# Kernel tuning notes

Measured on AMD Instinct MI355X. Metric: run time of the kernel, lower is better.

The kernel has to match this reference:

```python
import jax, jax.numpy as jnp
import numpy as np

BN_EPS = 1e-5


def setup_inputs() -> dict:
    key = jax.random.key(0)
    k_x, k_A, k_W, k_b = jax.random.split(key, 4)
    N, C_in, T, V = 32, 64, 300, 25
    P, C_out = 3, 128
    x = jax.random.normal(k_x, (N, C_in, T, V), dtype=jnp.float32)
    # adjacency partitions: nonnegative, row-normalized-ish (rand in [0,1))
    A = jax.random.uniform(k_A, (P, V, V), dtype=jnp.float32)
    # kaiming fan_in init for 1x1 conv weights: std = sqrt(2/fan_in)
    W = jax.random.normal(k_W, (P, C_out, C_in), dtype=jnp.float32) * np.sqrt(2.0 / C_in)
    b = jax.random.normal(k_b, (P, C_out), dtype=jnp.float32) * 0.01
    gamma = jnp.ones((C_out,), dtype=jnp.float32)
    beta = jnp.zeros((C_out,), dtype=jnp.float32)
    return {"x": x, "A": A, "W": W, "b": b, "gamma": gamma, "beta": beta}


def reference(x, A, W, b, gamma, beta):
    # x: (N, C, T, V); A: (P, V, V); W: (P, C_out, C_in); b: (P, C_out)
    # Per partition p: aggregate over graph (x @ A_p), then 1x1 conv, then sum over p.
    # Fused: y[n,o,t,v] = sum_p sum_c W[p,o,c] * (sum_w x[n,c,t,w] * A[p,w,v]) + sum_p b[p,o]
    xa = jnp.einsum('nctw,pwv->pnctv', x, A)            # (P, N, C_in, T, V)
    y = jnp.einsum('pnctv,poc->notv', xa, W)            # (N, C_out, T, V)
    y = y + jnp.sum(b, axis=0)[None, :, None, None]
    # BatchNorm2d, training-mode forward: stats over (N, T, V), biased variance
    mean = jnp.mean(y, axis=(0, 2, 3), keepdims=True)
    var = jnp.mean(jnp.square(y - mean), axis=(0, 2, 3), keepdims=True)
    y = (y - mean) * jax.lax.rsqrt(var + BN_EPS)
    y = y * gamma[None, :, None, None] + beta[None, :, None, None]
    return jax.nn.relu(y)
```

## Files before the change

kernel.cpp:

```cpp
#include <hip/hip_runtime.h>
#include <hip/hip_bf16.h>

#define NN 32
#define CIN 64
#define TTOT 300
#define VV 25
#define PP 3
#define COUT 128
#define TTILE 5
#define NTILES 60
#define CNT 240000.0f

#define XSTR 40
#define ZSTR 72
#define ZROWS 128

#define WS_STATS 0
#define WS_SCALE 256
#define WS_SHIFT 384
#define WS_BSUM  512
#define WS_W2    640

typedef float f32x4 __attribute__((ext_vector_type(4)));
typedef short s16x8 __attribute__((ext_vector_type(8)));

__device__ __forceinline__ short f2bf(float f) {
    unsigned u = __float_as_uint(f);
    u += 0x7fff + ((u >> 16) & 1);
    return (short)(u >> 16);
}

__global__ __launch_bounds__(256) void prep_kernel(const float* __restrict__ W,
                                                   const float* __restrict__ b,
                                                   float* __restrict__ ws) {
    int tid = blockIdx.x * blockDim.x + threadIdx.x;
    if (tid < 256) ws[WS_STATS + tid] = 0.0f;
    if (tid >= 256 && tid < 384) {
        int o = tid - 256;
        ws[WS_BSUM + o] = b[o] + b[COUT + o] + b[2 * COUT + o];
    }
    if (tid < COUT * 192) {
        int o = tid / 192, k = tid % 192;
        int p = k / 64, c = k % 64;
        ((short*)(ws + WS_W2))[tid] = f2bf(W[(p * COUT + o) * CIN + c]);
    }
}

__global__ __launch_bounds__(512, 4) void sgcn_main(const float* __restrict__ x,
                                                    const float* __restrict__ A,
                                                    float* __restrict__ y,
                                                    float* ws) {
    __shared__ __align__(16) short Xs[TTILE * 64 * XSTR];
    __shared__ __align__(16) short Ats[PP * 32 * XSTR];
    __shared__ __align__(16) short Z2s[ZROWS * ZSTR];
    __shared__ float sstat[256];
    const int tid  = threadIdx.x;
    const int lane = tid & 63;
    const int wave = tid >> 6;
    const int n  = blockIdx.x / NTILES;
    const int t0 = (blockIdx.x % NTILES) * TTILE;
    const int lg = lane >> 4;
    const int li = lane & 15;

    {
        const float* xb = x + (size_t)n * (CIN * TTOT * VV) + (size_t)t0 * VV;
        #pragma unroll
        for (int it = 0; it < 20; ++it) {
            int i = tid + it * 512;
            int c = i / 160;
            int r2 = i - c * 160;
            int t = r2 >> 5, w = r2 & 31;
            float val = (w < VV) ? xb[c * (TTOT * VV) + t * VV + w] : 0.0f;
            Xs[(t * 64 + c) * XSTR + w] = f2bf(val);
        }
        #pragma unroll
        for (int it = 0; it < 8; ++it) {
            int i = tid + it * 512;
            if (i < PP * 32 * XSTR) {
                int p = i / (32 * XSTR);
                int r = i - p * (32 * XSTR);
                int v = r / XSTR, w = r - v * XSTR;
                short val = (v < VV && w < VV) ? f2bf(A[p * (VV * VV) + w * VV + v])
                                               : (short)0;
                Ats[i] = val;
            }
        }
        if (tid < 108) ((int*)(Z2s + 125 * ZSTR))[tid] = 0;
        if (tid < 256) sstat[tid] = 0.0f;
    }
    __syncthreads();

    const int ow = wave >> 1;
    const int cw = wave & 1;
    const int o0 = ow * 32;
    const short* w2 = (const short*)(ws + WS_W2);

    f32x4 acc[2][4];
    #pragma unroll
    for (int mf = 0; mf < 2; ++mf)
        #pragma unroll
        for (int cf = 0; cf < 4; ++cf)
            acc[mf][cf] = (f32x4){0.f, 0.f, 0.f, 0.f};

    for (int p = 0; p < PP; ++p) {
        s16x8 wf[2][2];
        #pragma unroll
        for (int mf = 0; mf < 2; ++mf)
            #pragma unroll
            for (int ks = 0; ks < 2; ++ks)
                wf[mf][ks] = *(const s16x8*)(w2 + (o0 + mf * 16 + li) * 192
                                                + p * 64 + ks * 32 + lg * 8);

        #pragma unroll
        for (int q = 0; q < 5; ++q) {
            int f = wave * 5 + q;
            int t = f >> 3, rem = f & 7;
            int vf = rem >> 2, cfr = rem & 3;
            s16x8 af = *(const s16x8*)(&Ats[(p * 32 + vf * 16 + li) * XSTR + lg * 8]);
            s16x8 bf = *(const s16x8*)(&Xs[(t * 64 + cfr * 16 + li) * XSTR + lg * 8]);
            f32x4 z = (f32x4){0.f, 0.f, 0.f, 0.f};
            f32x4 d = __builtin_amdgcn_mfma_f32_16x16x32_bf16(af, bf, z, 0, 0, 0);
            int m0 = vf * 16 + lg * 4;
            int ccol = cfr * 16 + li;
            #pragma unroll
            for (int r = 0; r < 4; ++r) {
                int m = m0 + r;
                if (m < VV) Z2s[(t * VV + m) * ZSTR + ccol] = f2bf(d[r]);
            }
        }
        __syncthreads();

        #pragma unroll
        for (int cf = 0; cf < 4; ++cf) {
            int col0 = cw * 64 + cf * 16;
            #pragma unroll
            for (int ks = 0; ks < 2; ++ks) {
                s16x8 zf = *(const s16x8*)(&Z2s[(col0 + li) * ZSTR + ks * 32 + lg * 8]);
                #pragma unroll
                for (int mf = 0; mf < 2; ++mf)
                    acc[mf][cf] = __builtin_amdgcn_mfma_f32_16x16x32_bf16(
                        wf[mf][ks], zf, acc[mf][cf], 0, 0, 0);
            }
        }
        __syncthreads();
    }

    const float* bsum = ws + WS_BSUM;
    #pragma unroll
    for (int mf = 0; mf < 2; ++mf) {
        #pragma unroll
        for (int r = 0; r < 4; ++r) {
            int o = o0 + mf * 16 + lg * 4 + r;
            float bo = bsum[o];
            float s = 0.f, sq = 0.f;
            #pragma unroll
            for (int cf = 0; cf < 4; ++cf) {
                int col = cw * 64 + cf * 16 + li;
                float val = acc[mf][cf][r] + bo;
                if (col < TTILE * VV) {
                    y[(size_t)(n * COUT + o) * (TTOT * VV) + t0 * VV + col] = val;
                    s += val; sq += val * val;
                }
            }
            #pragma unroll
            for (int m = 1; m < 16; m <<= 1) {
                s  += __shfl_xor(s, m, 64);
                sq += __shfl_xor(sq, m, 64);
            }
            if (li == 0) {
                atomicAdd(&sstat[o], s);
                atomicAdd(&sstat[128 + o], sq);
            }
        }
    }
    __syncthreads();
    if (tid < 256) atomicAdd(&ws[WS_STATS + tid], sstat[tid]);
}

__global__ void finalize_kernel(const float* __restrict__ gamma,
                                const float* __restrict__ beta,
                                float* ws) {
    int o = threadIdx.x;
    float mean = ws[WS_STATS + o] * (1.0f / CNT);
    float ex2  = ws[WS_STATS + 128 + o] * (1.0f / CNT);
    float var  = ex2 - mean * mean;
    float rstd = rsqrtf(var + 1e-5f);
    float sc = gamma[o] * rstd;
    ws[WS_SCALE + o] = sc;
    ws[WS_SHIFT + o] = beta[o] - mean * sc;
}

__global__ __launch_bounds__(256) void norm_relu_kernel(float* __restrict__ y,
                                                        const float* __restrict__ ws) {
    const int total8 = (NN * COUT * TTOT * VV) / 8;
    const float* scale = ws + WS_SCALE;
    const float* shift = ws + WS_SHIFT;
    for (int i = blockIdx.x * blockDim.x + threadIdx.x; i < total8;
         i += gridDim.x * blockDim.x) {
        size_t base = (size_t)i * 8;
        int row0 = (int)(base / 7500);
        int row1 = (int)((base + 7) / 7500);
        int o0 = row0 & 127, o1 = row1 & 127;
        float s0 = scale[o0], h0 = shift[o0];
        float s1 = scale[o1], h1 = shift[o1];
        size_t bnd = (size_t)(row0 + 1) * 7500;
        float4 a = *(const float4*)(y + base);
        float4 b = *(const float4*)(y + base + 4);
        float vals[8] = {a.x, a.y, a.z, a.w, b.x, b.y, b.z, b.w};
        #pragma unroll
        for (int e = 0; e < 8; ++e) {
            bool first = (base + (size_t)e) < bnd;
            float s = first ? s0 : s1;
            float h = first ? h0 : h1;
            vals[e] = fmaxf(vals[e] * s + h, 0.0f);
        }
        a = make_float4(vals[0], vals[1], vals[2], vals[3]);
        b = make_float4(vals[4], vals[5], vals[6], vals[7]);
        *(float4*)(y + base) = a;
        *(float4*)(y + base + 4) = b;
    }
}

extern "C" void kernel_launch(void* const* d_in, const int* in_sizes, int n_in,
                              void* d_out, int out_size, void* d_ws, size_t ws_size,
                              hipStream_t stream) {
    const float* x     = (const float*)d_in[0];
    const float* A     = (const float*)d_in[1];
    const float* W     = (const float*)d_in[2];
    const float* b     = (const float*)d_in[3];
    const float* gamma = (const float*)d_in[4];
    const float* beta  = (const float*)d_in[5];
    float* y  = (float*)d_out;
    float* ws = (float*)d_ws;

    prep_kernel<<<96, 256, 0, stream>>>(W, b, ws);
    sgcn_main<<<NN * NTILES, 512, 0, stream>>>(x, A, y, ws);
    finalize_kernel<<<1, 128, 0, stream>>>(gamma, beta, ws);
    norm_relu_kernel<<<2048, 256, 0, stream>>>(y, ws);
}
```

Baseline: 148.6 us.

## Split fused graph-aggregation/conv kernel into two kernels through a bf16 workspace

Replaces the single fused kernel with an aggregation kernel that writes the x·A result as a bf16 column-major buffer (K=192 contiguous per column) into workspace, followed by a conv kernel that loads 128 columns via direct global-to-LDS loads with an XOR swizzle and runs a K=192 MFMA GEMM against preloaded weights. The intent is to drop the per-partition barriers and the low-utilisation 125-column tiles of the fused kernel, giving full 128-column tiles with all weights held in registers. In exchange it adds a round trip of roughly 92 MB of intermediate traffic, and it only takes effect when the workspace is large enough, falling back to the old kernel otherwise.

```diff
diff --git a/kernel.cpp b/kernel.cpp
--- a/kernel.cpp
+++ b/kernel.cpp
@@ -7,9 +7,11 @@
 #define VV 25
 #define PP 3
 #define COUT 128
+#define KTOT 192
 #define TTILE 5
 #define NTILES 60
 #define CNT 240000.0f
+#define NCOLS 240000
 
 #define XSTR 40
 #define ZSTR 72
@@ -20,6 +22,8 @@
 #define WS_SHIFT 384
 #define WS_BSUM  512
 #define WS_W2    640
+#define ZT_BYTE_OFF (1u << 20)
+#define WS_NEEDED (ZT_BYTE_OFF + (size_t)NCOLS * KTOT * 2)
 
 typedef float f32x4 __attribute__((ext_vector_type(4)));
 typedef short s16x8 __attribute__((ext_vector_type(8)));
@@ -28,6 +32,12 @@
     unsigned u = __float_as_uint(f);
     u += 0x7fff + ((u >> 16) & 1);
     return (short)(u >> 16);
+}
+
+__device__ __forceinline__ void gl_lds16(const void* g, void* l) {
+    __builtin_amdgcn_global_load_lds(
+        (const __attribute__((address_space(1))) unsigned int*)g,
+        (__attribute__((address_space(3))) unsigned int*)l, 16, 0, 0);
 }
 
 __global__ __launch_bounds__(256) void prep_kernel(const float* __restrict__ W,
@@ -39,10 +49,176 @@
         int o = tid - 256;
         ws[WS_BSUM + o] = b[o] + b[COUT + o] + b[2 * COUT + o];
     }
-    if (tid < COUT * 192) {
-        int o = tid / 192, k = tid % 192;
+    if (tid < COUT * KTOT) {
+        int o = tid / KTOT, k = tid % KTOT;
         int p = k / 64, c = k % 64;
         ((short*)(ws + WS_W2))[tid] = f2bf(W[(p * COUT + o) * CIN + c]);
+    }
+}
+
+
+__global__ __launch_bounds__(512, 4) void agg_kernel(const float* __restrict__ x,
+                                                     const float* __restrict__ A,
+                                                     short* __restrict__ Zt) {
+    __shared__ __align__(16) short Xs[TTILE * 64 * XSTR];
+    __shared__ __align__(16) short Ats[PP * 32 * XSTR];
+
+    const int tid  = threadIdx.x;
+    const int lane = tid & 63;
+    const int wave = tid >> 6;
+    const int n  = blockIdx.x / NTILES;
+    const int t0 = (blockIdx.x % NTILES) * TTILE;
+    const int lg = lane >> 4;
+    const int li = lane & 15;
+
+    {
+        const float* xb = x + (size_t)n * (CIN * TTOT * VV) + (size_t)t0 * VV;
+        #pragma unroll
+        for (int it = 0; it < 20; ++it) {
+            int i = tid + it * 512;
+            int c = i / 160;
+            int r2 = i - c * 160;
+            int t = r2 >> 5, w = r2 & 31;
+            float val = (w < VV) ? xb[c * (TTOT * VV) + t * VV + w] : 0.0f;
+            Xs[(t * 64 + c) * XSTR + w] = f2bf(val);
+        }
+        #pragma unroll
+        for (int it = 0; it < 8; ++it) {
+            int i = tid + it * 512;
+            if (i < PP * 32 * XSTR) {
+                int p = i / (32 * XSTR);
+                int r = i - p * (32 * XSTR);
+                int v = r / XSTR, w = r - v * XSTR;
+                Ats[i] = (v < VV && w < VV) ? f2bf(A[p * (VV * VV) + w * VV + v])
+                                            : (short)0;
+            }
+        }
+    }
+    __syncthreads();
+
+    const int cf = wave >> 1;
+    const int vf = wave & 1;
+    const int vv = vf * 16 + li;
+
+    s16x8 xa[TTILE];
+    #pragma unroll
+    for (int t = 0; t < TTILE; ++t)
+        xa[t] = *(const s16x8*)(&Xs[(t * 64 + cf * 16 + li) * XSTR + lg * 8]);
+    s16x8 af[PP];
+    #pragma unroll
+    for (int p = 0; p < PP; ++p)
+        af[p] = *(const s16x8*)(&Ats[(p * 32 + vf * 16 + li) * XSTR + lg * 8]);
+
+    const bool vok = (vv < VV);
+    const size_t colbase = (size_t)n * 7500 + (size_t)t0 * VV + vv;
+    #pragma unroll
+    for (int t = 0; t < TTILE; ++t) {
+        #pragma unroll
+        for (int p = 0; p < PP; ++p) {
+            f32x4 z = (f32x4){0.f, 0.f, 0.f, 0.f};
+            f32x4 d = __builtin_amdgcn_mfma_f32_16x16x32_bf16(xa[t], af[p], z, 0, 0, 0);
+            if (vok) {
+                ushort4 pk;
+                pk.x = (unsigned short)f2bf(d[0]);
+                pk.y = (unsigned short)f2bf(d[1]);
+                pk.z = (unsigned short)f2bf(d[2]);
+                pk.w = (unsigned short)f2bf(d[3]);
+                *(ushort4*)(&Zt[(colbase + (size_t)t * VV) * KTOT
+                                + p * 64 + cf * 16 + lg * 4]) = pk;
+            }
+        }
+    }
+}
+
+__global__ __launch_bounds__(512, 2) void conv_kernel(const short* __restrict__ Zt,
+                                                      float* __restrict__ y,
+                                                      float* ws) {
+    __shared__ __align__(16) short Zs[128 * KTOT];
+    const int tid  = threadIdx.x;
+    const int lane = tid & 63;
+    const int wave = tid >> 6;
+    const int lg = lane >> 4;
+    const int li = lane & 15;
+    const int c0 = blockIdx.x * 128;
+
+    {
+        const char* ztb = (const char*)Zt + (size_t)c0 * 384;
+        char* lbase = (char*)Zs + (size_t)wave * 64 * 16;
+        #pragma unroll
+        for (int it = 0; it < 6; ++it) {
+            int chunk = it * 512 + tid;
+            int col = chunk / 24;
+            int within = (chunk - col * 24) * 16;
+            int srcoff = within ^ ((col & 7) << 4);
+            gl_lds16(ztb + (size_t)col * 384 + srcoff, lbase + (size_t)it * 512 * 16);
+        }
+    }
+
+    const short* w2 = (const short*)(ws + WS_W2);
+    const int ow = wave >> 1;
+    const int ch = wave & 1;
+    const int o0 = ow * 32;
+    s16x8 wf[2][6];
+    #pragma unroll
+    for (int mf = 0; mf < 2; ++mf)
+        #pragma unroll
+        for (int ks = 0; ks < 6; ++ks)
+            wf[mf][ks] = *(const s16x8*)(w2 + (o0 + mf * 16 + li) * KTOT
+                                            + ks * 32 + lg * 8);
+
+    f32x4 acc[2][4];
+    #pragma unroll
+    for (int mf = 0; mf < 2; ++mf)
+        #pragma unroll
+        for (int cf = 0; cf < 4; ++cf)
+            acc[mf][cf] = (f32x4){0.f, 0.f, 0.f, 0.f};
+
+    __syncthreads();
+
+    #pragma unroll
+    for (int cf = 0; cf < 4; ++cf) {
+        int col = ch * 64 + cf * 16 + li;
+        int rb = col * 384;
+        int sw = (col & 7) << 4;
+        #pragma unroll
+        for (int ks = 0; ks < 6; ++ks) {
+            s16x8 zf = *(const s16x8*)((const char*)Zs
+                                       + ((rb + ks * 64 + lg * 16) ^ sw));
+            acc[0][cf] = __builtin_amdgcn_mfma_f32_16x16x32_bf16(wf[0][ks], zf,
+                                                                 acc[0][cf], 0, 0, 0);
+            acc[1][cf] = __builtin_amdgcn_mfma_f32_16x16x32_bf16(wf[1][ks], zf,
+                                                                 acc[1][cf], 0, 0, 0);
+        }
+    }
+
+    const float* bsum = ws + WS_BSUM;
+    float* stats = ws + WS_STATS;
+    #pragma unroll
+    for (int mf = 0; mf < 2; ++mf) {
+        #pragma unroll
+        for (int r = 0; r < 4; ++r) {
+            int o = o0 + mf * 16 + lg * 4 + r;
+            float bo = bsum[o];
+            float s = 0.f, sq = 0.f;
+            #pragma unroll
+            for (int cf = 0; cf < 4; ++cf) {
+                int col = c0 + ch * 64 + cf * 16 + li;
+                float val = acc[mf][cf][r] + bo;
+                int n = col / 7500;
+                int inner = col - n * 7500;
+                y[(size_t)(n * COUT + o) * 7500 + inner] = val;
+                s += val; sq += val * val;
+            }
+            #pragma unroll
+            for (int m = 1; m < 16; m <<= 1) {
+                s  += __shfl_xor(s, m, 64);
+                sq += __shfl_xor(sq, m, 64);
+            }
+            if (li == 0) {
+                atomicAdd(&stats[o], s);
+                atomicAdd(&stats[128 + o], sq);
+            }
+        }
     }
 }
 
@@ -54,6 +230,7 @@
     __shared__ __align__(16) short Ats[PP * 32 * XSTR];
     __shared__ __align__(16) short Z2s[ZROWS * ZSTR];
     __shared__ float sstat[256];
+
     const int tid  = threadIdx.x;
     const int lane = tid & 63;
     const int wave = tid >> 6;
@@ -80,9 +257,8 @@
                 int p = i / (32 * XSTR);
                 int r = i - p * (32 * XSTR);
                 int v = r / XSTR, w = r - v * XSTR;
-                short val = (v < VV && w < VV) ? f2bf(A[p * (VV * VV) + w * VV + v])
-                                               : (short)0;
-                Ats[i] = val;
+                Ats[i] = (v < VV && w < VV) ? f2bf(A[p * (VV * VV) + w * VV + v])
+                                            : (short)0;
             }
         }
         if (tid < 108) ((int*)(Z2s + 125 * ZSTR))[tid] = 0;
@@ -103,14 +279,13 @@
             acc[mf][cf] = (f32x4){0.f, 0.f, 0.f, 0.f};
 
     for (int p = 0; p < PP; ++p) {
-        s16x8 wf[2][2];
+        s16x8 wfl[2][2];
         #pragma unroll
         for (int mf = 0; mf < 2; ++mf)
             #pragma unroll
             for (int ks = 0; ks < 2; ++ks)
-                wf[mf][ks] = *(const s16x8*)(w2 + (o0 + mf * 16 + li) * 192
-                                                + p * 64 + ks * 32 + lg * 8);
-
+                wfl[mf][ks] = *(const s16x8*)(w2 + (o0 + mf * 16 + li) * KTOT
+                                                 + p * 64 + ks * 32 + lg * 8);
         #pragma unroll
         for (int q = 0; q < 5; ++q) {
             int f = wave * 5 + q;
@@ -129,7 +304,6 @@
             }
         }
         __syncthreads();
-
         #pragma unroll
         for (int cf = 0; cf < 4; ++cf) {
             int col0 = cw * 64 + cf * 16;
@@ -139,7 +313,7 @@
                 #pragma unroll
                 for (int mf = 0; mf < 2; ++mf)
                     acc[mf][cf] = __builtin_amdgcn_mfma_f32_16x16x32_bf16(
-                        wf[mf][ks], zf, acc[mf][cf], 0, 0, 0);
+                        wfl[mf][ks], zf, acc[mf][cf], 0, 0, 0);
             }
         }
         __syncthreads();
@@ -234,7 +408,13 @@
     float* ws = (float*)d_ws;
 
     prep_kernel<<<96, 256, 0, stream>>>(W, b, ws);
-    sgcn_main<<<NN * NTILES, 512, 0, stream>>>(x, A, y, ws);
+    if (ws_size >= WS_NEEDED) {
+        short* Zt = (short*)((char*)d_ws + ZT_BYTE_OFF);
+        agg_kernel<<<NN * NTILES, 512, 0, stream>>>(x, A, Zt);
+        conv_kernel<<<NCOLS / 128, 512, 0, stream>>>(Zt, y, ws);
+    } else {
+        sgcn_main<<<NN * NTILES, 512, 0, stream>>>(x, A, y, ws);
+    }
     finalize_kernel<<<1, 128, 0, stream>>>(gamma, beta, ws);
     norm_relu_kernel<<<2048, 256, 0, stream>>>(y, ws);
 }
```

After: 479.0 us. 222% more time.
